# Optimization experiments

Hardware: AMD Instinct MI355X
Metric: run time of the kernel (lower is better)

Reference implementation:

```python
import jax, jax.numpy as jnp
import numpy as np

N_QUBITS = 8
N_LAYERS = 2
BATCH = 16384
INPUT_DIM = 3072
NUM_CLASSES = 10

I2 = np.eye(2, dtype=np.complex64)
PAULIS = [
    I2,
    np.array([[0, 1], [1, 0]], np.complex64),      # X
    np.array([[0, -1j], [1j, 0]], np.complex64),   # Y
    np.array([[1, 0], [0, -1]], np.complex64),     # Z
]
XX = np.kron(PAULIS[1], PAULIS[1])
YY = np.kron(PAULIS[2], PAULIS[2])
ZZ = np.kron(PAULIS[3], PAULIS[3])
I4 = np.eye(4, dtype=np.complex64)


def u3(p):
    # PennyLane U3(theta, phi, lambda)
    th, ph, lam = p[0], p[1], p[2]
    c = jnp.cos(th / 2).astype(jnp.complex64)
    s = jnp.sin(th / 2).astype(jnp.complex64)
    return jnp.stack([
        jnp.stack([c, -jnp.exp(1j * lam) * s]),
        jnp.stack([jnp.exp(1j * ph) * s, jnp.exp(1j * (ph + lam)) * c]),
    ])


def cu3(p):
    U = u3(p)
    Z = jnp.zeros((2, 2), U.dtype)
    Ic = jnp.asarray(I2)
    top = jnp.concatenate([Ic, Z], axis=1)
    bot = jnp.concatenate([Z, U], axis=1)
    return jnp.concatenate([top, bot], axis=0)


def ising(P, phi):
    # exp(-i phi/2 * P) with P a 2-qubit Pauli word (P^2 = I)
    return jnp.cos(phi / 2) * I4 - 1j * jnp.sin(phi / 2) * P


def apply_1q(psi, U, w):
    psi = jnp.moveaxis(psi, 1 + w, -1)
    psi = jnp.einsum('ij,...j->...i', U, psi)
    return jnp.moveaxis(psi, -1, 1 + w)


def apply_2q(psi, U, a, b):
    psi = jnp.moveaxis(psi, (1 + a, 1 + b), (-2, -1))
    sh = psi.shape
    psi = jnp.einsum('ij,...j->...i', U, psi.reshape(sh[:-2] + (4,)))
    return jnp.moveaxis(psi.reshape(sh), (-2, -1), (1 + a, 1 + b))


def apply_ry_batched(psi, theta, w):
    # per-sample RY angle (AngleEmbedding, rotation='Y')
    c = jnp.cos(theta / 2).reshape((-1,) + (1,) * (psi.ndim - 2))
    s = jnp.sin(theta / 2).reshape((-1,) + (1,) * (psi.ndim - 2))
    psi = jnp.moveaxis(psi, 1 + w, -1)
    a0, a1 = psi[..., 0], psi[..., 1]
    psi = jnp.stack([c * a0 - s * a1, s * a0 + c * a1], axis=-1)
    return jnp.moveaxis(psi, -1, 1 + w)


def dilated_conv(psi, W, wires):
    n = len(wires)
    if n == 8:
        pairs = [(0, 2), (1, 3), (4, 6), (5, 7)]
    elif n == 4:
        pairs = [(0, 2), (1, 3)]
    elif n == 2:
        pairs = [(0, 1)]
    else:
        pairs = [(i, i + 2) for i in range(n - 2)]
    processed = set()
    for q1, q2 in pairs:
        if q1 in wires and q2 in wires:
            psi = apply_1q(psi, u3(W[q1, 0:3]), q1)
            psi = apply_1q(psi, u3(W[q2, 3:6]), q2)
            psi = apply_2q(psi, ising(ZZ, W[q1, 6]), q1, q2)
            psi = apply_2q(psi, ising(YY, W[q1, 7]), q1, q2)
            psi = apply_2q(psi, ising(XX, W[q1, 8]), q1, q2)
            psi = apply_1q(psi, u3(W[q1, 9:12]), q1)
            psi = apply_1q(psi, u3(W[q2, 12:15]), q2)
            processed.update((q1, q2))
    for w in wires:
        if w not in processed:
            for i in range(5):
                psi = apply_1q(psi, u3(W[w, 3 * i:3 * i + 3]), w)
    return psi


def pooling(psi, P, wires):
    for indx, w in enumerate(wires):
        if indx % 2 == 1:
            # measure wire w, cond-U3 on wires[indx-1]; deferred -> CU3(ctrl=w, tgt=wires[indx-1])
            psi = apply_2q(psi, cu3(P[indx // 2]), w, wires[indx - 1])
    return psi


def _gray_pauli_words(k):
    # matches pennylane _n_k_gray_code(4, k) ordering, identity word dropped
    words = []
    for i in range(4 ** k):
        br = []
        v = i
        for _ in range(k):
            br.append(v % 4)
            v //= 4
        cw = [0] * k
        shift = 0
        for j in reversed(range(k)):
            cw[j] = (br[j] + shift) % 4
            shift += 4 - cw[j]
        if any(cw):
            words.append(tuple(cw))
    return words


def arbitrary_unitary(psi, weights, wires):
    # qml.ArbitraryUnitary: sequence of PauliRot(weights[i], word) gates
    k = len(wires)
    Ik = np.eye(2 ** k, dtype=np.complex64)
    for idx, cw in enumerate(_gray_pauli_words(k)):
        P = np.array([[1.0]], np.complex64)
        for p in cw:
            P = np.kron(P, PAULIS[p])
        th = weights[idx]
        G = jnp.cos(th / 2) * Ik - 1j * jnp.sin(th / 2) * P
        psi = apply_2q(psi, G, wires[0], wires[1])
    return psi


def run_circuit(features, conv, pool, last):
    B = features.shape[0]
    psi = jnp.zeros((B, 2 ** N_QUBITS), jnp.complex64).at[:, 0].set(1.0)
    psi = psi.reshape((B,) + (2,) * N_QUBITS)
    for w in range(N_QUBITS):
        psi = apply_ry_batched(psi, features[:, w], w)
    wires = list(range(N_QUBITS))
    for layer in range(N_LAYERS):
        psi = dilated_conv(psi, conv[layer], wires)
        psi = pooling(psi, pool[layer], wires)
        wires = wires[::2]
    psi = arbitrary_unitary(psi, last, wires)
    probs = psi.real ** 2 + psi.imag ** 2
    z0 = probs[:, 0].reshape(B, -1).sum(-1) - probs[:, 1].reshape(B, -1).sum(-1)
    return z0  # <Z_0> per sample


def setup_inputs():
    key = jax.random.key(0)
    ks = jax.random.split(key, 8)
    return {
        'x': jax.random.normal(ks[0], (BATCH, INPUT_DIM), jnp.float32),
        'fc_w': jax.random.normal(ks[1], (N_QUBITS, INPUT_DIM), jnp.float32) * 0.02,
        'fc_b': jnp.zeros((N_QUBITS,), jnp.float32),
        'conv_params': jax.random.normal(ks[2], (N_LAYERS, N_QUBITS, 15), jnp.float32),
        'pool_params': jax.random.normal(ks[3], (N_LAYERS, N_QUBITS // 2, 3), jnp.float32),
        'last_params': jax.random.normal(ks[4], (15,), jnp.float32),
        'fc_out_w': jax.random.normal(ks[5], (NUM_CLASSES, 1), jnp.float32),
        'fc_out_b': jnp.zeros((NUM_CLASSES,), jnp.float32),
    }


def reference(x, fc_w, fc_b, conv_params, pool_params, last_params, fc_out_w, fc_out_b):
    reduced = jnp.tanh(x @ fc_w.T + fc_b)                      # (B, n_qubits)
    z0 = run_circuit(reduced, conv_params, pool_params, last_params)  # (B,)
    logits = z0[:, None] * fc_out_w[:, 0][None, :] + fc_out_b  # (B, num_classes)
    return logits
```

## Files before the change

kernel.cpp:

```cpp
#include <hip/hip_runtime.h>
#include <math.h>

__device__ inline float2 cmul(float2 a, float2 b){
  return make_float2(a.x*b.x - a.y*b.y, a.x*b.y + a.y*b.x);
}

__device__ inline void mk_u3(const float* p, float2& u00, float2& u01, float2& u10, float2& u11){
  float s, c;   sincosf(0.5f*p[0], &s, &c);
  float sl, cl; sincosf(p[1], &sl, &cl);
  float sm, cm; sincosf(p[2], &sm, &cm);
  float s2, c2; sincosf(p[1] + p[2], &s2, &c2);
  u00 = make_float2(c, 0.f);
  u01 = make_float2(-s*cm, -s*sm);
  u10 = make_float2( s*cl,  s*sl);
  u11 = make_float2( c*c2,  c*s2);
}

__device__ inline void pauli2(int t, float2* m){
  if (t == 0){ m[0]=make_float2(1,0); m[1]=make_float2(0,0);  m[2]=make_float2(0,0); m[3]=make_float2(1,0); }
  else if (t == 1){ m[0]=make_float2(0,0); m[1]=make_float2(1,0);  m[2]=make_float2(1,0); m[3]=make_float2(0,0); }
  else if (t == 2){ m[0]=make_float2(0,0); m[1]=make_float2(0,-1); m[2]=make_float2(0,1); m[3]=make_float2(0,0); }
  else            { m[0]=make_float2(1,0); m[1]=make_float2(0,0);  m[2]=make_float2(0,0); m[3]=make_float2(-1,0);}
}

struct GSpec { int type; int w1; int w2; int poff; };
#define NG 66
__device__ const GSpec gspec[NG] = {
  {0,0,0,  0},{0,2,0, 33},{1,0,2,  6},{2,0,2,  7},{3,0,2,  8},{0,0,0,  9},{0,2,0, 42},
  {0,1,0, 15},{0,3,0, 48},{1,1,3, 21},{2,1,3, 22},{3,1,3, 23},{0,1,0, 24},{0,3,0, 57},
  {0,4,0, 60},{0,6,0, 93},{1,4,6, 66},{2,4,6, 67},{3,4,6, 68},{0,4,0, 69},{0,6,0,102},
  {0,5,0, 75},{0,7,0,108},{1,5,7, 81},{2,5,7, 82},{3,5,7, 83},{0,5,0, 84},{0,7,0,117},
  {4,1,0,1000},{4,3,2,1003},{4,5,4,1006},{4,7,6,1009},
  {0,0,0,120},{0,2,0,153},{1,0,2,126},{2,0,2,127},{3,0,2,128},{0,0,0,129},{0,2,0,162},
  {0,4,0,180},{0,4,0,183},{0,4,0,186},{0,4,0,189},{0,4,0,192},
  {0,6,0,210},{0,6,0,213},{0,6,0,216},{0,6,0,219},{0,6,0,222},
  {4,2,0,1012},{4,6,4,1015},
  {5,1,0,2000},{5,2,0,2001},{5,3,0,2002},{5,3,1,2003},{5,0,1,2004},
  {5,1,1,2005},{5,2,1,2006},{5,2,2,2007},{5,3,2,2008},{5,0,2,2009},
  {5,1,2,2010},{5,1,3,2011},{5,2,3,2012},{5,3,3,2013},{5,0,3,2014},
};

__device__ inline void apply1q(float2* S, int lane, int bit,
                               float2 u00, float2 u01, float2 u10, float2 u11){
  #pragma unroll
  for (int t = 0; t < 2; t++){
    int p  = lane + 64*t;
    int k0 = ((p >> bit) << (bit+1)) | (p & ((1<<bit)-1));
    int k1 = k0 | (1 << bit);
    float2 a = S[k0], b = S[k1];
    float2 na = make_float2(u00.x*a.x - u00.y*a.y + u01.x*b.x - u01.y*b.y,
                            u00.x*a.y + u00.y*a.x + u01.x*b.y + u01.y*b.x);
    float2 nb = make_float2(u10.x*a.x - u10.y*a.y + u11.x*b.x - u11.y*b.y,
                            u10.x*a.y + u10.y*a.x + u11.x*b.y + u11.y*b.x);
    S[k0] = na; S[k1] = nb;
  }
  __syncthreads();
}

__device__ inline void apply2q(float2* S, int lane, int bitA, int bitB, const float2* G){
  int hi = bitA > bitB ? bitA : bitB;
  int lo = bitA ^ bitB ^ hi;
  int t2  = ((lane >> lo) << (lo+1)) | (lane & ((1<<lo)-1));
  int k00 = ((t2   >> hi) << (hi+1)) | (t2   & ((1<<hi)-1));
  int mA = 1 << bitA, mB = 1 << bitB;
  int id[4] = { k00, k00|mB, k00|mA, k00|mA|mB };
  float2 v[4];
  #pragma unroll
  for (int r = 0; r < 4; r++) v[r] = S[id[r]];
  #pragma unroll
  for (int r = 0; r < 4; r++){
    float re = 0.f, im = 0.f;
    #pragma unroll
    for (int c = 0; c < 4; c++){
      float2 g = G[r*4 + c];
      re += g.x*v[c].x - g.y*v[c].y;
      im += g.x*v[c].y + g.y*v[c].x;
    }
    S[id[r]] = make_float2(re, im);
  }
  __syncthreads();
}

__global__ __launch_bounds__(64) void kern_sim(const float* __restrict__ conv,
                                               const float* __restrict__ pool,
                                               const float* __restrict__ last,
                                               float2* __restrict__ U){
  __shared__ float2 Gt[NG*16];
  __shared__ float2 S[256];
  const int lane = threadIdx.x;
  const int j = blockIdx.x;

  for (int g = lane; g < NG; g += 64){
    GSpec sp = gspec[g];
    const float* base;
    if (sp.poff >= 2000)      base = last + (sp.poff - 2000);
    else if (sp.poff >= 1000) base = pool + (sp.poff - 1000);
    else                      base = conv + sp.poff;
    float2 G[16];
    #pragma unroll
    for (int i = 0; i < 16; i++) G[i] = make_float2(0.f, 0.f);
    if (sp.type == 0){
      float2 a,b,c,d; mk_u3(base,a,b,c,d);
      G[0]=a; G[1]=b; G[2]=c; G[3]=d;
    } else if (sp.type == 1){
      float s,co; sincosf(0.5f*base[0], &s, &co);
      G[0]=make_float2(co,-s); G[5]=make_float2(co,s); G[10]=make_float2(co,s); G[15]=make_float2(co,-s);
    } else if (sp.type == 2){
      float s,co; sincosf(0.5f*base[0], &s, &co);
      G[0]=G[5]=G[10]=G[15]=make_float2(co,0.f);
      G[3]=make_float2(0.f,s); G[6]=make_float2(0.f,-s); G[9]=make_float2(0.f,-s); G[12]=make_float2(0.f,s);
    } else if (sp.type == 3){
      float s,co; sincosf(0.5f*base[0], &s, &co);
      G[0]=G[5]=G[10]=G[15]=make_float2(co,0.f);
      G[3]=G[6]=G[9]=G[12]=make_float2(0.f,-s);
    } else if (sp.type == 4){
      float2 a,b,c,d; mk_u3(base,a,b,c,d);
      G[0]=make_float2(1.f,0.f); G[5]=make_float2(1.f,0.f);
      G[10]=a; G[11]=b; G[14]=c; G[15]=d;
    } else {
      float s,co; sincosf(0.5f*base[0], &s, &co);
      float2 A2[4], B2[4]; pauli2(sp.w1,A2); pauli2(sp.w2,B2);
      #pragma unroll
      for (int i1 = 0; i1 < 2; i1++)
      #pragma unroll
      for (int i2 = 0; i2 < 2; i2++)
      #pragma unroll
      for (int j1 = 0; j1 < 2; j1++)
      #pragma unroll
      for (int j2 = 0; j2 < 2; j2++){
        float2 Pv = cmul(A2[i1*2+j1], B2[i2*2+j2]);
        int rr = i1*2+i2, cc = j1*2+j2;
        G[rr*4+cc] = make_float2((rr==cc ? co : 0.f) + s*Pv.y, -s*Pv.x);
      }
    }
    #pragma unroll
    for (int i = 0; i < 16; i++) Gt[g*16 + i] = G[i];
  }
  #pragma unroll
  for (int t = 0; t < 4; t++){ int k = lane + 64*t; S[k] = make_float2(k==j ? 1.f : 0.f, 0.f); }
  __syncthreads();

  for (int g = 0; g < NG; g++){
    GSpec sp = gspec[g];
    if (sp.type == 0){
      float2 a = Gt[g*16+0], b = Gt[g*16+1], c = Gt[g*16+2], d = Gt[g*16+3];
      apply1q(S, lane, 7 - sp.w1, a, b, c, d);
    } else {
      int bA, bB;
      if (sp.type == 5){ bA = 7; bB = 3; }
      else             { bA = 7 - sp.w1; bB = 7 - sp.w2; }
      apply2q(S, lane, bA, bB, &Gt[g*16]);
    }
  }
  #pragma unroll
  for (int t = 0; t < 4; t++){ int k = lane + 64*t; U[k*256 + j] = S[k]; }
}

__global__ __launch_bounds__(256) void kern_m2(const float2* __restrict__ U,
                                               float* __restrict__ mt){
  __shared__ float dsh[256];
  const int xm = blockIdx.x, i = threadIdx.x;
  const int j2 = i ^ xm;
  float acc = 0.f;
  #pragma unroll 4
  for (int k = 0; k < 128; k++){
    float2 ui0 = U[k*256 + i];
    float2 uj0 = U[k*256 + j2];
    float2 ui1 = U[(k+128)*256 + i];
    float2 uj1 = U[(k+128)*256 + j2];
    acc += (ui0.x*uj0.x + ui0.y*uj0.y) - (ui1.x*uj1.x + ui1.y*uj1.y);
  }
  dsh[i] = acc;
  __syncthreads();
  for (int bit = 1; bit < 256; bit <<= 1){
    float mine = dsh[i], other = dsh[i ^ bit];
    __syncthreads();
    dsh[i] = (i & bit) ? (other - mine) : (mine + other);
    __syncthreads();
  }
  if ((i & xm) == 0){
    int idx = 0, pw = 1;
    #pragma unroll
    for (int b2 = 0; b2 < 8; b2++){
      int dg = ((xm >> b2) & 1) ? 1 : (((i >> b2) & 1) ? 2 : 0);
      idx += dg * pw; pw *= 3;
    }
    mt[idx] = dsh[i] * (1.0f/256.0f);
  }
}

__global__ __launch_bounds__(256) void kern_gemv(const float* __restrict__ x,
                                                 const float* __restrict__ w,
                                                 const float* __restrict__ b,
                                                 float* __restrict__ red){
  const int wave = threadIdx.x >> 6, lane = threadIdx.x & 63;
  const int rg = lane >> 4, co = lane & 15;
  const int rowb = blockIdx.x*64 + wave*16 + rg*4;
  const float4* xp0 = (const float4*)(x + (size_t)(rowb+0)*3072);
  const float4* xp1 = (const float4*)(x + (size_t)(rowb+1)*3072);
  const float4* xp2 = (const float4*)(x + (size_t)(rowb+2)*3072);
  const float4* xp3 = (const float4*)(x + (size_t)(rowb+3)*3072);
  const float4* wp = (const float4*)w;
  float acc[8][4];
  #pragma unroll
  for (int q = 0; q < 8; q++)
    #pragma unroll
    for (int r = 0; r < 4; r++) acc[q][r] = 0.f;
  for (int it = 0; it < 48; it++){
    int c = it*16 + co;
    float4 xv0 = xp0[c], xv1 = xp1[c], xv2 = xp2[c], xv3 = xp3[c];
    #pragma unroll
    for (int q = 0; q < 8; q++){
      float4 wv = wp[q*768 + c];
      acc[q][0] += wv.x*xv0.x + wv.y*xv0.y + wv.z*xv0.z + wv.w*xv0.w;
      acc[q][1] += wv.x*xv1.x + wv.y*xv1.y + wv.z*xv1.z + wv.w*xv1.w;
      acc[q][2] += wv.x*xv2.x + wv.y*xv2.y + wv.z*xv2.z + wv.w*xv2.w;
      acc[q][3] += wv.x*xv3.x + wv.y*xv3.y + wv.z*xv3.z + wv.w*xv3.w;
    }
  }
  #pragma unroll
  for (int q = 0; q < 8; q++)
    #pragma unroll
    for (int r = 0; r < 4; r++){
      float v = acc[q][r];
      v += __shfl_xor(v, 1);
      v += __shfl_xor(v, 2);
      v += __shfl_xor(v, 4);
      v += __shfl_xor(v, 8);
      acc[q][r] = v;
    }
  if (co == 0){
    #pragma unroll
    for (int r = 0; r < 4; r++){
      int row = rowb + r;
      float4 o0 = make_float4(tanhf(acc[0][r]+b[0]), tanhf(acc[1][r]+b[1]),
                              tanhf(acc[2][r]+b[2]), tanhf(acc[3][r]+b[3]));
      float4 o1 = make_float4(tanhf(acc[4][r]+b[4]), tanhf(acc[5][r]+b[5]),
                              tanhf(acc[6][r]+b[6]), tanhf(acc[7][r]+b[7]));
      float4* rp = (float4*)(red + (size_t)row*8);
      rp[0] = o0; rp[1] = o1;
    }
  }
}

__global__ __launch_bounds__(256) void kern_contract(const float* __restrict__ red,
                                                     const float* __restrict__ mt,
                                                     const float* __restrict__ fow,
                                                     const float* __restrict__ fob,
                                                     float* __restrict__ out){
  __shared__ float mtl[9*27*32];
  __shared__ float zsh[4*64];
  const int tid = threadIdx.x;
  for (int idx = tid; idx < 9*27*32; idx += 256){
    int h  = idx / 864;
    int r  = idx - h*864;
    int mm = r >> 5, l = r & 31;
    mtl[idx] = (l < 27) ? mt[h*729 + mm*27 + l] : 0.f;
  }
  const int wave = tid >> 6, lane = tid & 63;
  const int e = blockIdx.x*64 + lane;
  const float4* rp = (const float4*)(red + (size_t)e*8);
  float4 r0 = rp[0], r1 = rp[1];
  __syncthreads();

  float rr[8] = {r0.x, r0.y, r0.z, r0.w, r1.x, r1.y, r1.z, r1.w};
  float sn[8], cs[8];
  #pragma unroll
  for (int q = 0; q < 8; q++) sincosf(rr[q], &sn[q], &cs[q]);
  float f0[3] = {1.f, sn[7], cs[7]};
  float f1[3] = {1.f, sn[6], cs[6]};
  float f2[3] = {1.f, sn[5], cs[5]};
  float g27[32];
  #pragma unroll
  for (int z = 27; z < 32; z++) g27[z] = 0.f;
  #pragma unroll
  for (int d2 = 0; d2 < 3; d2++)
  #pragma unroll
  for (int d1 = 0; d1 < 3; d1++)
  #pragma unroll
  for (int d0 = 0; d0 < 3; d0++)
    g27[9*d2 + 3*d1 + d0] = f2[d2]*f1[d1]*f0[d0];
  float4 glo4[8];
  #pragma unroll
  for (int v = 0; v < 8; v++)
    glo4[v] = make_float4(g27[4*v], g27[4*v+1], g27[4*v+2], g27[4*v+3]);
  float f3[3] = {1.f, sn[4], cs[4]};
  float f4[3] = {1.f, sn[3], cs[3]};
  float f5[3] = {1.f, sn[2], cs[2]};
  float gmid[27];
  #pragma unroll
  for (int d5 = 0; d5 < 3; d5++)
  #pragma unroll
  for (int d4 = 0; d4 < 3; d4++)
  #pragma unroll
  for (int d3 = 0; d3 < 3; d3++)
    gmid[9*d5 + 3*d4 + d3] = f5[d5]*f4[d4]*f3[d3];
  float f6[3] = {1.f, sn[1], cs[1]};
  float f7[3] = {1.f, sn[0], cs[0]};
  float ghi[9];
  #pragma unroll
  for (int d7 = 0; d7 < 3; d7++)
  #pragma unroll
  for (int d6 = 0; d6 < 3; d6++)
    ghi[3*d7 + d6] = f7[d7]*f6[d6];

  const int hbeg = (wave==0) ? 0 : (wave==1) ? 3 : (wave==2) ? 5 : 7;
  const int hend = hbeg + ((wave==0) ? 3 : 2);
  float part = 0.f;
  for (int h = hbeg; h < hend; h++){
    float ha = 0.f, hb = 0.f;
    #pragma unroll 3
    for (int mm = 0; mm < 27; mm++){
      const float4* mp = (const float4*)&mtl[(h*27 + mm) << 5];
      float d0 = 0.f, d1 = 0.f;
      #pragma unroll
      for (int v = 0; v < 8; v += 2){
        float4 m0 = mp[v], m1 = mp[v+1];
        d0 += m0.x*glo4[v].x   + m0.y*glo4[v].y   + m0.z*glo4[v].z   + m0.w*glo4[v].w;
        d1 += m1.x*glo4[v+1].x + m1.y*glo4[v+1].y + m1.z*glo4[v+1].z + m1.w*glo4[v+1].w;
      }
      float term = (d0 + d1) * gmid[mm];
      if (mm & 1) hb += term; else ha += term;
    }
    part += (ha + hb) * ghi[h];
  }
  zsh[wave*64 + lane] = part;
  __syncthreads();

  for (int idx = tid; idx < 640; idx += 256){
    int el = idx / 10, c = idx - el*10;
    float z = zsh[el] + zsh[64+el] + zsh[128+el] + zsh[192+el];
    out[((size_t)blockIdx.x*64 + el)*10 + c] = z*fow[c] + fob[c];
  }
}

extern "C" void kernel_launch(void* const* d_in, const int* in_sizes, int n_in,
                              void* d_out, int out_size, void* d_ws, size_t ws_size,
                              hipStream_t stream) {
  (void)in_sizes; (void)n_in; (void)out_size; (void)ws_size;
  const float* x    = (const float*)d_in[0];
  const float* fcw  = (const float*)d_in[1];
  const float* fcb  = (const float*)d_in[2];
  const float* conv = (const float*)d_in[3];
  const float* pool = (const float*)d_in[4];
  const float* last = (const float*)d_in[5];
  const float* fow  = (const float*)d_in[6];
  const float* fob  = (const float*)d_in[7];
  float* out = (float*)d_out;

  char* ws = (char*)d_ws;
  float2* U   = (float2*)ws;
  float*  red = (float*) (ws + 512*1024);
  float*  mt  = (float*) (ws + 1024*1024);

  kern_sim     <<<256, 64,  0, stream>>>(conv, pool, last, U);
  kern_m2      <<<256, 256, 0, stream>>>(U, mt);
  kern_gemv    <<<256, 256, 0, stream>>>(x, fcw, fcb, red);
  kern_contract<<<256, 256, 0, stream>>>(red, mt, fow, fob, out);
}
```

Before: 391.5 us.

## Remap GEMV to two rows per wave and launch more blocks

```diff
diff --git a/kernel.cpp b/kernel.cpp
--- a/kernel.cpp
+++ b/kernel.cpp
@@ -189,57 +189,45 @@
   }
 }
 
-__global__ __launch_bounds__(256) void kern_gemv(const float* __restrict__ x,
-                                                 const float* __restrict__ w,
-                                                 const float* __restrict__ b,
-                                                 float* __restrict__ red){
+__global__ __launch_bounds__(256, 8) void kern_gemv(const float* __restrict__ x,
+                                                    const float* __restrict__ w,
+                                                    const float* __restrict__ b,
+                                                    float* __restrict__ red){
   const int wave = threadIdx.x >> 6, lane = threadIdx.x & 63;
-  const int rg = lane >> 4, co = lane & 15;
-  const int rowb = blockIdx.x*64 + wave*16 + rg*4;
-  const float4* xp0 = (const float4*)(x + (size_t)(rowb+0)*3072);
-  const float4* xp1 = (const float4*)(x + (size_t)(rowb+1)*3072);
-  const float4* xp2 = (const float4*)(x + (size_t)(rowb+2)*3072);
-  const float4* xp3 = (const float4*)(x + (size_t)(rowb+3)*3072);
+  const int rl = lane >> 5, co = lane & 31;
+  const int gw = blockIdx.x*4 + wave;
+  const int row = gw*2 + rl;
+  const float4* xp = (const float4*)(x + (size_t)row*3072);
   const float4* wp = (const float4*)w;
-  float acc[8][4];
-  #pragma unroll
-  for (int q = 0; q < 8; q++)
-    #pragma unroll
-    for (int r = 0; r < 4; r++) acc[q][r] = 0.f;
-  for (int it = 0; it < 48; it++){
-    int c = it*16 + co;
-    float4 xv0 = xp0[c], xv1 = xp1[c], xv2 = xp2[c], xv3 = xp3[c];
+  float acc[8];
+  #pragma unroll
+  for (int q = 0; q < 8; q++) acc[q] = 0.f;
+  for (int it = 0; it < 24; it++){
+    int c = it*32 + co;
+    float4 xv = xp[c];
     #pragma unroll
     for (int q = 0; q < 8; q++){
       float4 wv = wp[q*768 + c];
-      acc[q][0] += wv.x*xv0.x + wv.y*xv0.y + wv.z*xv0.z + wv.w*xv0.w;
-      acc[q][1] += wv.x*xv1.x + wv.y*xv1.y + wv.z*xv1.z + wv.w*xv1.w;
-      acc[q][2] += wv.x*xv2.x + wv.y*xv2.y + wv.z*xv2.z + wv.w*xv2.w;
-      acc[q][3] += wv.x*xv3.x + wv.y*xv3.y + wv.z*xv3.z + wv.w*xv3.w;
-    }
-  }
-  #pragma unroll
-  for (int q = 0; q < 8; q++)
-    #pragma unroll
-    for (int r = 0; r < 4; r++){
-      float v = acc[q][r];
-      v += __shfl_xor(v, 1);
-      v += __shfl_xor(v, 2);
-      v += __shfl_xor(v, 4);
-      v += __shfl_xor(v, 8);
-      acc[q][r] = v;
-    }
+      acc[q] += wv.x*xv.x + wv.y*xv.y + wv.z*xv.z + wv.w*xv.w;
+    }
+  }
+  #pragma unroll
+  for (int q = 0; q < 8; q++){
+    float v = acc[q];
+    v += __shfl_xor(v, 1);
+    v += __shfl_xor(v, 2);
+    v += __shfl_xor(v, 4);
+    v += __shfl_xor(v, 8);
+    v += __shfl_xor(v, 16);
+    acc[q] = v;
+  }
   if (co == 0){
-    #pragma unroll
-    for (int r = 0; r < 4; r++){
-      int row = rowb + r;
-      float4 o0 = make_float4(tanhf(acc[0][r]+b[0]), tanhf(acc[1][r]+b[1]),
-                              tanhf(acc[2][r]+b[2]), tanhf(acc[3][r]+b[3]));
-      float4 o1 = make_float4(tanhf(acc[4][r]+b[4]), tanhf(acc[5][r]+b[5]),
-                              tanhf(acc[6][r]+b[6]), tanhf(acc[7][r]+b[7]));
-      float4* rp = (float4*)(red + (size_t)row*8);
-      rp[0] = o0; rp[1] = o1;
-    }
+    float4 o0 = make_float4(tanhf(acc[0]+b[0]), tanhf(acc[1]+b[1]),
+                            tanhf(acc[2]+b[2]), tanhf(acc[3]+b[3]));
+    float4 o1 = make_float4(tanhf(acc[4]+b[4]), tanhf(acc[5]+b[5]),
+                            tanhf(acc[6]+b[6]), tanhf(acc[7]+b[7]));
+    float4* rp = (float4*)(red + (size_t)row*8);
+    rp[0] = o0; rp[1] = o1;
   }
 }
 
@@ -353,8 +341,8 @@
   float*  red = (float*) (ws + 512*1024);
   float*  mt  = (float*) (ws + 1024*1024);
 
-  kern_sim     <<<256, 64,  0, stream>>>(conv, pool, last, U);
-  kern_m2      <<<256, 256, 0, stream>>>(U, mt);
-  kern_gemv    <<<256, 256, 0, stream>>>(x, fcw, fcb, red);
-  kern_contract<<<256, 256, 0, stream>>>(red, mt, fow, fob, out);
-}
+  kern_sim     <<<256,  64,  0, stream>>>(conv, pool, last, U);
+  kern_m2      <<<256,  256, 0, stream>>>(U, mt);
+  kern_gemv    <<<2048, 256, 0, stream>>>(x, fcw, fcb, red);
+  kern_contract<<<256,  256, 0, stream>>>(red, mt, fow, fob, out);
+}
```

Result: slower. 407.4 us (+4.1%).
